# Optimization experiments

Hardware: AMD Instinct MI355X
Metric: run time of the kernel (lower is better)

## Reference

```python
import itertools
import jax, jax.numpy as jnp
import numpy as np

B, N, C, H = 4, 48, 16, 64
CIN = [48, 64, 128, 192]   # per-order MLP input dims after expand/reduce/concat/permute
COUT = 16

def _exclude_mask(n, cnt, dtype):
    # mask[i1..icnt] = 1 iff all object indices are pairwise distinct
    if cnt <= 1:
        return jnp.ones((n,), dtype=dtype)
    idx = [jnp.arange(n).reshape((1,) * d + (n,) + (1,) * (cnt - 1 - d)) for d in range(cnt)]
    m = jnp.ones((n,) * cnt, dtype=bool)
    for a in range(cnt):
        for b in range(a + 1, cnt):
            m = m & (idx[a] != idx[b])
    return m.astype(dtype)

def _reduce(x, dim):
    # x: [B] + [n]*dim + [C]; exists=max / forall=min over last object axis, exclude_self mask
    n = x.shape[1]
    m = _exclude_mask(n, dim, x.dtype)[..., None]  # [n]*dim + [1], broadcasts over B and C
    ex = jnp.max(x * m, axis=-2)
    fa = jnp.min(x * m + (1.0 - m), axis=-2)
    out = jnp.stack([ex, fa], axis=-1)  # interleave (exists, forall) per channel
    return out.reshape(out.shape[:-2] + (out.shape[-2] * 2,))

def _expand(x, dim, n):
    # insert a new object axis at position dim+1 and broadcast to n
    return jnp.broadcast_to(jnp.expand_dims(x, dim + 1), x.shape[:dim + 1] + (n,) + x.shape[dim + 1:])

def _permute(x, dim):
    # concat all permutations of the object axes along channels
    if dim <= 1:
        return x
    parts = [jnp.transpose(x, (0,) + p + (dim + 1,)) for p in itertools.permutations(range(1, dim + 1))]
    return jnp.concatenate(parts, axis=-1)

def _logic(x, W1, b1, W2, b2):
    # LogicInferenceLayer: Linear -> ReLU -> Linear -> Sigmoid on channel axis
    return jax.nn.sigmoid(jax.nn.relu(x @ W1 + b1) @ W2 + b2)

def setup_inputs() -> dict:
    key = jax.random.key(0)
    ks = jax.random.split(key, 24)
    inp = {
        'x0': jax.random.uniform(ks[0], (B, C), dtype=jnp.float32),
        'x1': jax.random.uniform(ks[1], (B, N, C), dtype=jnp.float32),
        'x2': jax.random.uniform(ks[2], (B, N, N, C), dtype=jnp.float32),
        'x3': jax.random.uniform(ks[3], (B, N, N, N, C), dtype=jnp.float32),
    }
    for o, cin in enumerate(CIN):
        inp[f'W1_{o}'] = jax.random.normal(ks[4 + 4 * o], (cin, H), dtype=jnp.float32) * 0.05
        inp[f'b1_{o}'] = jnp.zeros((H,), dtype=jnp.float32)
        inp[f'W2_{o}'] = jax.random.normal(ks[5 + 4 * o], (H, COUT), dtype=jnp.float32) * 0.05
        inp[f'b2_{o}'] = jnp.zeros((COUT,), dtype=jnp.float32)
    return inp

def reference(x0, x1, x2, x3,
              W1_0, b1_0, W2_0, b2_0,
              W1_1, b1_1, W2_1, b2_1,
              W1_2, b1_2, W2_2, b2_2,
              W1_3, b1_3, W2_3, b2_3):
    n = x1.shape[1]
    # order 0: [self, reduce(order1)]
    t0 = jnp.concatenate([x0, _reduce(x1, 1)], axis=-1)
    y0 = _logic(t0, W1_0, b1_0, W2_0, b2_0)
    # order 1: [expand(order0), self, reduce(order2)]
    t1 = jnp.concatenate([_expand(x0, 0, n), x1, _reduce(x2, 2)], axis=-1)
    y1 = _logic(t1, W1_1, b1_1, W2_1, b2_1)
    # order 2: [expand(order1), self, reduce(order3)], permute 2 object axes
    t2 = jnp.concatenate([_expand(x1, 1, n), x2, _reduce(x3, 3)], axis=-1)
    y2 = _logic(_permute(t2, 2), W1_2, b1_2, W2_2, b2_2)
    # order 3 (max order): [expand(order2), self], permute 3 object axes
    t3 = jnp.concatenate([_expand(x2, 2, n), x3], axis=-1)
    y3 = _logic(_permute(t3, 3), W1_3, b1_3, W2_3, b2_3)
    return (y0, y1, y2, y3)
```

## Files before the change

### kernel.cpp

```cpp
#include <hip/hip_runtime.h>
#include <hip/hip_bf16.h>


typedef __bf16 bf16x8 __attribute__((ext_vector_type(8)));
typedef unsigned short us8 __attribute__((ext_vector_type(8)));
typedef float f32x4 __attribute__((ext_vector_type(4)));

#define NPAIR 589824
#define NRED3 294912
#define NX3   7077888

__device__ __forceinline__ unsigned short f2bf(float f) {
    __hip_bfloat16 h = __float2bfloat16(f);
    return __builtin_bit_cast(unsigned short, h);
}
__device__ __forceinline__ unsigned int pk2(float a, float b) {
    return (unsigned int)f2bf(a) | ((unsigned int)f2bf(b) << 16);
}
__device__ __forceinline__ float bflo(unsigned int u) {
    return __builtin_bit_cast(float, u << 16);
}
__device__ __forceinline__ float bfhi(unsigned int u) {
    return __builtin_bit_cast(float, u & 0xffff0000u);
}
__device__ __forceinline__ float sigmoidf_(float z) {
    return 1.0f / (1.0f + __expf(-z));
}
__device__ __forceinline__ bf16x8 ld_bf8(const unsigned short* p) {
    return __builtin_bit_cast(bf16x8, *(const us8*)p);
}
__device__ __forceinline__ bf16x8 pack8(float4 a, float4 b) {
    us8 u;
    u[0] = f2bf(a.x); u[1] = f2bf(a.y); u[2] = f2bf(a.z); u[3] = f2bf(a.w);
    u[4] = f2bf(b.x); u[5] = f2bf(b.y); u[6] = f2bf(b.z); u[7] = f2bf(b.w);
    return __builtin_bit_cast(bf16x8, u);
}

__global__ __launch_bounds__(192) void perm3_kernel(
    const float* __restrict__ x3,
    unsigned short* __restrict__ X0, unsigned short* __restrict__ XA,
    unsigned short* __restrict__ XB, unsigned short* __restrict__ red3)
{
    __shared__ float rowf[768];
    const int g = blockIdx.x;
    const int m2 = g % 48, t1 = g / 48, m1 = t1 % 48, b = t1 / 48;
    const int t = threadIdx.x;
    const int m3 = t >> 2, cq = (t & 3) * 4;
    const float4 v = *(const float4*)(x3 + (size_t)g * 768 + m3 * 16 + cq);
    *(float4*)(rowf + m3 * 16 + cq) = v;
    const uint2 u = make_uint2(pk2(v.x, v.y), pk2(v.z, v.w));
    *(uint2*)(X0 + (size_t)g * 768 + m3 * 16 + cq) = u;
    *(uint2*)(XA + (((size_t)(b * 48 + m1) * 48 + m3) * 48 + m2) * 16 + cq) = u;
    *(uint2*)(XB + (((size_t)(b * 48 + m2) * 48 + m3) * 48 + m1) * 16 + cq) = u;
    __syncthreads();
    if (t < 16) {
        const int c = t;
        float ex = -__builtin_inff(), fa = __builtin_inff();
        const bool mij = (m1 != m2);
#pragma unroll 8
        for (int k = 0; k < 48; ++k) {
            const bool m = mij & (k != m1) & (k != m2);
            const float vv = rowf[k * 16 + c];
            ex = fmaxf(ex, m ? vv : 0.f);
            fa = fminf(fa, m ? vv : 1.f);
        }
        *(unsigned int*)(red3 + (size_t)g * 32 + 2 * c) = pk2(ex, fa);
    }
}

__global__ __launch_bounds__(256) void phaseA_kernel(
    const float* __restrict__ x2, const float* __restrict__ W1,
    const float* __restrict__ b1,
    float* __restrict__ wsA, unsigned short* __restrict__ wsB,
    unsigned short* __restrict__ wsC)
{
    __shared__ float xr[4][32];
    const int t = threadIdx.x;
    if (t < 128) {
        const int pr2 = t >> 5, c = t & 31;
        const int gg = blockIdx.x * 4 + pr2;
        const int bb = gg / 2304, pp2 = gg % 2304, P = pp2 / 48, Q = pp2 % 48;
        const float* base = x2 + (size_t)bb * 36864;
        xr[pr2][c] = (c < 16) ? base[(P * 48 + Q) * 16 + c]
                              : base[(Q * 48 + P) * 16 + (c - 16)];
    }
    __syncthreads();
    const int pr = t >> 6, h = t & 63;
    const int g = blockIdx.x * 4 + pr;
    float a = b1[h], bacc = 0.f, cacc = 0.f;
#pragma unroll
    for (int c = 0; c < 16; ++c) {
        const float xpq = xr[pr][c], xqp = xr[pr][16 + c];
        a    += xpq * W1[(  0 + c) * 64 + h] + xqp * W1[( 64 + c) * 64 + h];
        bacc += xpq * W1[( 32 + c) * 64 + h] + xqp * W1[( 96 + c) * 64 + h];
        cacc += xpq * W1[(128 + c) * 64 + h] + xqp * W1[(160 + c) * 64 + h];
    }
    const size_t o = (size_t)g * 64 + h;
    wsA[o] = a;
    wsB[o] = f2bf(bacc);
    wsC[o] = f2bf(cacc);
}

#define Y3_TILES 8

__global__ __launch_bounds__(192, 3) void y3_kernel(
    const unsigned short* __restrict__ X0,
    const unsigned short* __restrict__ XA,
    const unsigned short* __restrict__ XB,
    const float* __restrict__ W1, const float* __restrict__ W2,
    const float* __restrict__ b2,
    const float* __restrict__ wsA,
    const unsigned short* __restrict__ wsB,
    const unsigned short* __restrict__ wsC,
    float* __restrict__ out)
{
    __shared__ __align__(16) unsigned short w1t[64 * 104];
    const int t = threadIdx.x;
    const int w = t >> 6, lane = t & 63, lr = lane & 15, lg = lane >> 4;

#pragma unroll
    for (int p = 0; p < 16; ++p) {
        const int e = p * 192 + t;
        const int h = e & 63, kk = (e >> 6) * 2;
        const int r0 = 16 + ((kk >> 4) << 5) + (kk & 15);
        *(unsigned int*)(w1t + h * 104 + kk) =
            pk2(W1[r0 * 64 + h], W1[(r0 + 1) * 64 + h]);
    }
    __syncthreads();

    bf16x8 w1f[4][3];
#pragma unroll
    for (int n = 0; n < 4; ++n)
#pragma unroll
        for (int ks = 0; ks < 3; ++ks)
            w1f[n][ks] = ld_bf8(w1t + (16 * n + lr) * 104 + 32 * ks + 8 * lg);

    bf16x8 w2f[2];
#pragma unroll
    for (int m = 0; m < 2; ++m) {
        us8 u;
#pragma unroll
        for (int e = 0; e < 8; ++e) {
            const int ch = 16 * (e >> 1) + 4 * lg + 2 * (e & 1) + m;
            u[e] = f2bf(W2[ch * 16 + lr]);
        }
        w2f[m] = __builtin_bit_cast(bf16x8, u);
    }
    const float4 b2v = *(const float4*)(b2 + 4 * lg);
    const int row = 16 * w + lr;
    const int roff = row * 16 + 8 * (lg & 1);
    const bool hi = (lg >> 1) != 0;

    const int g0 = blockIdx.x * Y3_TILES;
    const int b = g0 / 2304, pp = g0 % 2304, i = pp / 48, j0 = pp % 48;

    const size_t baseB = ((size_t)((b * 48 + i) * 48 + row)) * 64 + 4 * lg;
    uint2 Bu[4];
#pragma unroll
    for (int n = 0; n < 4; ++n) Bu[n] = *(const uint2*)(wsB + baseB + 16 * n);

    const size_t rowIJ = ((size_t)(b * 48 + i) * 48) * 768;

    bf16x8 xc0, xc1, xc2;
    uint2 Cu[4];
    {
        const size_t bIJ = rowIJ + (size_t)j0 * 768;
        const size_t bJI = ((size_t)(b * 48 + j0) * 48 + i) * 768;
        xc0 = ld_bf8((hi ? XA + bIJ : X0 + bIJ) + roff);
        xc1 = ld_bf8((hi ? XB + bIJ : X0 + bJI) + roff);
        xc2 = ld_bf8((hi ? XB + bJI : XA + bJI) + roff);
        const size_t baseC = ((size_t)((b * 48 + j0) * 48 + row)) * 64 + 4 * lg;
#pragma unroll
        for (int n = 0; n < 4; ++n) Cu[n] = *(const uint2*)(wsC + baseC + 16 * n);
    }

#pragma unroll
    for (int it = 0; it < Y3_TILES; ++it) {
        const int j = j0 + it;
        bf16x8 xn0, xn1, xn2;
        uint2 Cn[4];
        if (it < Y3_TILES - 1) {
            const int jn = j + 1;
            const size_t bIJ = rowIJ + (size_t)jn * 768;
            const size_t bJI = ((size_t)(b * 48 + jn) * 48 + i) * 768;
            xn0 = ld_bf8((hi ? XA + bIJ : X0 + bIJ) + roff);
            xn1 = ld_bf8((hi ? XB + bIJ : X0 + bJI) + roff);
            xn2 = ld_bf8((hi ? XB + bJI : XA + bJI) + roff);
            const size_t baseC = ((size_t)((b * 48 + jn) * 48 + row)) * 64 + 4 * lg;
#pragma unroll
            for (int n = 0; n < 4; ++n) Cn[n] = *(const uint2*)(wsC + baseC + 16 * n);
        }
        f32x4 acc[4];
#pragma unroll
        for (int n = 0; n < 4; ++n) {
            acc[n] = f32x4{0.f, 0.f, 0.f, 0.f};
            acc[n] = __builtin_amdgcn_mfma_f32_16x16x32_bf16(w1f[n][0], xc0, acc[n], 0, 0, 0);
            acc[n] = __builtin_amdgcn_mfma_f32_16x16x32_bf16(w1f[n][1], xc1, acc[n], 0, 0, 0);
            acc[n] = __builtin_amdgcn_mfma_f32_16x16x32_bf16(w1f[n][2], xc2, acc[n], 0, 0, 0);
        }
        const size_t baseA = ((size_t)((b * 48 + i) * 48 + j)) * 64 + 4 * lg;
#pragma unroll
        for (int n = 0; n < 4; ++n) {
            const float4 Au = *(const float4*)(wsA + baseA + 16 * n);
            acc[n][0] = fmaxf(acc[n][0] + Au.x + bflo(Bu[n].x) + bflo(Cu[n].x), 0.f);
            acc[n][1] = fmaxf(acc[n][1] + Au.y + bfhi(Bu[n].x) + bfhi(Cu[n].x), 0.f);
            acc[n][2] = fmaxf(acc[n][2] + Au.z + bflo(Bu[n].y) + bflo(Cu[n].y), 0.f);
            acc[n][3] = fmaxf(acc[n][3] + Au.w + bfhi(Bu[n].y) + bfhi(Cu[n].y), 0.f);
        }
        bf16x8 hf[2];
#pragma unroll
        for (int m = 0; m < 2; ++m) {
            us8 u;
#pragma unroll
            for (int e = 0; e < 8; ++e)
                u[e] = f2bf(acc[e >> 1][2 * (e & 1) + m]);
            hf[m] = __builtin_bit_cast(bf16x8, u);
        }
        f32x4 o2 = {0.f, 0.f, 0.f, 0.f};
        o2 = __builtin_amdgcn_mfma_f32_16x16x32_bf16(w2f[0], hf[0], o2, 0, 0, 0);
        o2 = __builtin_amdgcn_mfma_f32_16x16x32_bf16(w2f[1], hf[1], o2, 0, 0, 0);
        float4 ov;
        ov.x = sigmoidf_(o2[0] + b2v.x);
        ov.y = sigmoidf_(o2[1] + b2v.y);
        ov.z = sigmoidf_(o2[2] + b2v.z);
        ov.w = sigmoidf_(o2[3] + b2v.w);
        *(float4*)(out + (size_t)(g0 + it) * 768 + row * 16 + 4 * lg) = ov;
        if (it < Y3_TILES - 1) {
            xc0 = xn0; xc1 = xn1; xc2 = xn2;
#pragma unroll
            for (int n = 0; n < 4; ++n) Cu[n] = Cn[n];
        }
    }
}

__global__ __launch_bounds__(192, 3) void y3_gather_kernel(
    const float* __restrict__ x3,
    const float* __restrict__ W1, const float* __restrict__ W2,
    const float* __restrict__ b2,
    const float* __restrict__ wsA,
    const unsigned short* __restrict__ wsB,
    const unsigned short* __restrict__ wsC,
    float* __restrict__ out)
{
    __shared__ __align__(16) unsigned short w1t[64 * 104];
    const int t = threadIdx.x;
    const int w = t >> 6, lane = t & 63, lr = lane & 15, lg = lane >> 4;
#pragma unroll
    for (int p = 0; p < 16; ++p) {
        const int e = p * 192 + t;
        const int h = e & 63, kk = (e >> 6) * 2;
        const int r0 = 16 + ((kk >> 4) << 5) + (kk & 15);
        *(unsigned int*)(w1t + h * 104 + kk) =
            pk2(W1[r0 * 64 + h], W1[(r0 + 1) * 64 + h]);
    }
    __syncthreads();
    bf16x8 w1f[4][3];
#pragma unroll
    for (int n = 0; n < 4; ++n)
#pragma unroll
        for (int ks = 0; ks < 3; ++ks)
            w1f[n][ks] = ld_bf8(w1t + (16 * n + lr) * 104 + 32 * ks + 8 * lg);
    bf16x8 w2f[2];
#pragma unroll
    for (int m = 0; m < 2; ++m) {
        us8 u;
// ... 65 lines not shown
        *(float4*)(out + (size_t)g * 768 + row * 16 + 4 * lg) = ov;
    }
}

__global__ __launch_bounds__(256) void red3_kernel(
    const float* __restrict__ x3, unsigned short* __restrict__ red3)
{
    const int slot = blockIdx.x * 256 + threadIdx.x;
    const int c = slot & 15;
    const int q = slot >> 4;
    const int j = q % 48, pi = q / 48, i = pi % 48;
    const float* p = x3 + (size_t)q * 768 + c;
    float ex = -__builtin_inff(), fa = __builtin_inff();
    const bool mij = (i != j);
#pragma unroll 8
    for (int k = 0; k < 48; ++k) {
        const bool m = mij & (k != i) & (k != j);
        const float v = p[k * 16];
        ex = fmaxf(ex, m ? v : 0.f);
        fa = fminf(fa, m ? v : 1.f);
    }
    *(unsigned int*)(red3 + (size_t)q * 32 + 2 * c) = pk2(ex, fa);
}

__global__ __launch_bounds__(192, 3) void y2_mlp_kernel(
    const float* __restrict__ x1, const float* __restrict__ x2,
    const float* __restrict__ W1, const float* __restrict__ b1,
    const float* __restrict__ W2, const float* __restrict__ b2,
    const unsigned short* __restrict__ red3, float* __restrict__ out)
{
    __shared__ __align__(16) unsigned short w1t[64 * 136];
    const int t = threadIdx.x;
    const int w = t >> 6, lane = t & 63, lr = lane & 15, lg = lane >> 4;

#pragma unroll
    for (int p = 0; p < 22; ++p) {
        const int e = p * 192 + t;
        if (e < 4096) {
            const int h = e & 63, k2 = e >> 6;
            *(unsigned int*)(w1t + h * 136 + 2 * k2) =
                pk2(W1[(2 * k2) * 64 + h], W1[(2 * k2 + 1) * 64 + h]);
        }
    }
    __syncthreads();

    bf16x8 w1f[4][4];
#pragma unroll
    for (int n = 0; n < 4; ++n)
#pragma unroll
        for (int ks = 0; ks < 4; ++ks)
            w1f[n][ks] = ld_bf8(w1t + (16 * n + lr) * 136 + 32 * ks + 8 * lg);

    bf16x8 w2f[2];
#pragma unroll
    for (int m = 0; m < 2; ++m) {
        us8 u;
#pragma unroll
        for (int e = 0; e < 8; ++e) {
            const int ch = 16 * (e >> 1) + 4 * lg + 2 * (e & 1) + m;
            u[e] = f2bf(W2[ch * 16 + lr]);
        }
        w2f[m] = __builtin_bit_cast(bf16x8, u);
    }
    float4 b1v[4];
#pragma unroll
    for (int n = 0; n < 4; ++n) b1v[n] = *(const float4*)(b1 + 16 * n + 4 * lg);
    const float4 b2v = *(const float4*)(b2 + 4 * lg);

    const int bq = blockIdx.x;
    const int b = bq / 48, i = bq % 48;
    const float* x2b = x2 + (size_t)b * 36864;
    const int row = 16 * w + lr;
    const int j = row;
    const int c0 = 8 * (lg & 1);
    const bool hi = (lg >> 1) != 0;

    const float* a0 = hi ? (x2b + (i * 48 + j) * 16 + c0) : (x1 + (b * 48 + i) * 16 + c0);
    const float* a2 = hi ? (x2b + (j * 48 + i) * 16 + c0) : (x1 + (b * 48 + j) * 16 + c0);
    const unsigned short* r1 = red3 + ((size_t)(b * 48 + i) * 48 + j) * 32 + (hi ? 16 : 0) + c0;
    const unsigned short* r3 = red3 + ((size_t)(b * 48 + j) * 48 + i) * 32 + (hi ? 16 : 0) + c0;

    const bf16x8 xf0 = pack8(*(const float4*)a0, *(const float4*)(a0 + 4));
    const bf16x8 xf1 = ld_bf8(r1);
    const bf16x8 xf2 = pack8(*(const float4*)a2, *(const float4*)(a2 + 4));
    const bf16x8 xf3 = ld_bf8(r3);

    f32x4 acc[4];
#pragma unroll
    for (int n = 0; n < 4; ++n) {
        acc[n] = f32x4{0.f, 0.f, 0.f, 0.f};
        acc[n] = __builtin_amdgcn_mfma_f32_16x16x32_bf16(w1f[n][0], xf0, acc[n], 0, 0, 0);
        acc[n] = __builtin_amdgcn_mfma_f32_16x16x32_bf16(w1f[n][1], xf1, acc[n], 0, 0, 0);
        acc[n] = __builtin_amdgcn_mfma_f32_16x16x32_bf16(w1f[n][2], xf2, acc[n], 0, 0, 0);
        acc[n] = __builtin_amdgcn_mfma_f32_16x16x32_bf16(w1f[n][3], xf3, acc[n], 0, 0, 0);
    }
#pragma unroll
    for (int n = 0; n < 4; ++n) {
        acc[n][0] = fmaxf(acc[n][0] + b1v[n].x, 0.f);
        acc[n][1] = fmaxf(acc[n][1] + b1v[n].y, 0.f);
        acc[n][2] = fmaxf(acc[n][2] + b1v[n].z, 0.f);
        acc[n][3] = fmaxf(acc[n][3] + b1v[n].w, 0.f);
    }
    bf16x8 hf[2];
#pragma unroll
    for (int m = 0; m < 2; ++m) {
        us8 u;
#pragma unroll
        for (int e = 0; e < 8; ++e)
            u[e] = f2bf(acc[e >> 1][2 * (e & 1) + m]);
        hf[m] = __builtin_bit_cast(bf16x8, u);
    }
    f32x4 o2 = {0.f, 0.f, 0.f, 0.f};
    o2 = __builtin_amdgcn_mfma_f32_16x16x32_bf16(w2f[0], hf[0], o2, 0, 0, 0);
    o2 = __builtin_amdgcn_mfma_f32_16x16x32_bf16(w2f[1], hf[1], o2, 0, 0, 0);
    float4 ov;
    ov.x = sigmoidf_(o2[0] + b2v.x);
    ov.y = sigmoidf_(o2[1] + b2v.y);
    ov.z = sigmoidf_(o2[2] + b2v.z);
    ov.w = sigmoidf_(o2[3] + b2v.w);
// ... 10 lines not shown
    float* __restrict__ out)
{
    const int t = threadIdx.x;
    if (blockIdx.x < 4) {
        __shared__ __align__(16) unsigned short w1t[64 * 72];
        __shared__ __align__(16) unsigned short red2l[48 * 32];
        const int b = blockIdx.x;
#pragma unroll
        for (int p = 0; p < 11; ++p) {
            const int e = p * 192 + t;
            if (e < 2048) {
                const int h = e & 63, k2 = e >> 6;
                *(unsigned int*)(w1t + h * 72 + 2 * k2) =
                    pk2(W1_1[(2 * k2) * 64 + h], W1_1[(2 * k2 + 1) * 64 + h]);
            }
        }
        const float* x2b = x2 + (size_t)b * 36864;
#pragma unroll
        for (int s4 = 0; s4 < 4; ++s4) {
            const int s = t + 192 * s4;
            const int i = s >> 4, c = s & 15;
            const float* p = x2b + i * 768 + c;
            float ex = -__builtin_inff(), fa = __builtin_inff();
#pragma unroll 8
            for (int jj = 0; jj < 48; ++jj) {
                const bool m = (jj != i);
                const float v = p[jj * 16];
                ex = fmaxf(ex, m ? v : 0.f);
                fa = fminf(fa, m ? v : 1.f);
            }
            *(unsigned int*)(red2l + i * 32 + 2 * c) = pk2(ex, fa);
        }
        __syncthreads();

        const int w = t >> 6, lane = t & 63, lr = lane & 15, lg = lane >> 4;
        const int i = 16 * w + lr;
        const int rho = b * 48 + i;
        bf16x8 w1f[4][2];
#pragma unroll
        for (int n = 0; n < 4; ++n)
#pragma unroll
            for (int ks = 0; ks < 2; ++ks)
                w1f[n][ks] = ld_bf8(w1t + (16 * n + lr) * 72 + 32 * ks + 8 * lg);
        bf16x8 w2f[2];
#pragma unroll
        for (int m = 0; m < 2; ++m) {
            us8 u;
#pragma unroll
            for (int e = 0; e < 8; ++e) {
                const int ch = 16 * (e >> 1) + 4 * lg + 2 * (e & 1) + m;
                u[e] = f2bf(W2_1[ch * 16 + lr]);
            }
            w2f[m] = __builtin_bit_cast(bf16x8, u);
        }
        float4 b1v[4];
#pragma unroll
        for (int n = 0; n < 4; ++n) b1v[n] = *(const float4*)(b1_1 + 16 * n + 4 * lg);
        const float4 b2v = *(const float4*)(b2_1 + 4 * lg);

        const int c0 = 8 * (lg & 1);
        const float* a0 = (lg < 2) ? (x0 + b * 16 + c0) : (x1 + rho * 16 + c0);
        const bf16x8 xf0 = pack8(*(const float4*)a0, *(const float4*)(a0 + 4));
        const bf16x8 xf1 = ld_bf8(red2l + i * 32 + 8 * lg);

        f32x4 acc[4];
#pragma unroll
        for (int n = 0; n < 4; ++n) {
            acc[n] = f32x4{0.f, 0.f, 0.f, 0.f};
            acc[n] = __builtin_amdgcn_mfma_f32_16x16x32_bf16(w1f[n][0], xf0, acc[n], 0, 0, 0);
            acc[n] = __builtin_amdgcn_mfma_f32_16x16x32_bf16(w1f[n][1], xf1, acc[n], 0, 0, 0);
        }
#pragma unroll
        for (int n = 0; n < 4; ++n) {
            acc[n][0] = fmaxf(acc[n][0] + b1v[n].x, 0.f);
            acc[n][1] = fmaxf(acc[n][1] + b1v[n].y, 0.f);
            acc[n][2] = fmaxf(acc[n][2] + b1v[n].z, 0.f);
            acc[n][3] = fmaxf(acc[n][3] + b1v[n].w, 0.f);
        }
        bf16x8 hf[2];
#pragma unroll
        for (int m = 0; m < 2; ++m) {
            us8 u;
#pragma unroll
            for (int e = 0; e < 8; ++e)
                u[e] = f2bf(acc[e >> 1][2 * (e & 1) + m]);
            hf[m] = __builtin_bit_cast(bf16x8, u);
        }
        f32x4 o2 = {0.f, 0.f, 0.f, 0.f};
        o2 = __builtin_amdgcn_mfma_f32_16x16x32_bf16(w2f[0], hf[0], o2, 0, 0, 0);
        o2 = __builtin_amdgcn_mfma_f32_16x16x32_bf16(w2f[1], hf[1], o2, 0, 0, 0);
        float4 ov;
        ov.x = sigmoidf_(o2[0] + b2v.x);
        ov.y = sigmoidf_(o2[1] + b2v.y);
        ov.z = sigmoidf_(o2[2] + b2v.z);
        ov.w = sigmoidf_(o2[3] + b2v.w);
        *(float4*)(out + 64 + (size_t)rho * 16 + 4 * lg) = ov;
    } else {
// ... 230 lines not shown
extern "C" void kernel_launch(void* const* d_in, const int* in_sizes, int n_in,
                              void* d_out, int out_size, void* d_ws, size_t ws_size,
                              hipStream_t stream) {
    (void)in_sizes; (void)n_in; (void)out_size;
    const float* x0 = (const float*)d_in[0];
    const float* x1 = (const float*)d_in[1];
    const float* x2 = (const float*)d_in[2];
    const float* x3 = (const float*)d_in[3];
    const float* W1_0 = (const float*)d_in[4];
    const float* b1_0 = (const float*)d_in[5];
    const float* W2_0 = (const float*)d_in[6];
    const float* b2_0 = (const float*)d_in[7];
    const float* W1_1 = (const float*)d_in[8];
    const float* b1_1 = (const float*)d_in[9];
    const float* W2_1 = (const float*)d_in[10];
    const float* b2_1 = (const float*)d_in[11];
    const float* W1_2 = (const float*)d_in[12];
    const float* b1_2 = (const float*)d_in[13];
    const float* W2_2 = (const float*)d_in[14];
    const float* b2_2 = (const float*)d_in[15];
    const float* W1_3 = (const float*)d_in[16];
    const float* b1_3 = (const float*)d_in[17];
    const float* W2_3 = (const float*)d_in[18];
    const float* b2_3 = (const float*)d_in[19];
    float* out = (float*)d_out;

    const size_t ws_mid  = (size_t)8 * NPAIR + (size_t)2 * NRED3;
    const size_t ws_full = ws_mid + (size_t)6 * NX3;
    if (ws_size >= ws_mid) {
        float* wsA = (float*)d_ws;
        unsigned short* wsB = (unsigned short*)d_ws + 2 * NPAIR;
        unsigned short* wsC = wsB + NPAIR;
        unsigned short* red3 = (unsigned short*)d_ws + 4 * NPAIR;
        phaseA_kernel<<<2304, 256, 0, stream>>>(x2, W1_3, b1_3, wsA, wsB, wsC);
        if (ws_size >= ws_full) {
            unsigned short* X0 = red3 + NRED3;
            unsigned short* XA = X0 + NX3;
            unsigned short* XB = XA + NX3;
            perm3_kernel<<<9216, 192, 0, stream>>>(x3, X0, XA, XB, red3);
            y3_kernel<<<9216 / Y3_TILES, 192, 0, stream>>>(
                X0, XA, XB, W1_3, W2_3, b2_3, wsA, wsB, wsC, out + 150592);
        } else {
            y3_gather_kernel<<<2304, 192, 0, stream>>>(x3, W1_3, W2_3, b2_3,
                                                       wsA, wsB, wsC, out + 150592);
            red3_kernel<<<576, 256, 0, stream>>>(x3, red3);
        }
        y2_mlp_kernel<<<192, 192, 0, stream>>>(x1, x2, W1_2, b1_2, W2_2, b2_2,
                                               red3, out + 3136);
    } else {
        y3_fallback_kernel<<<1024, 192, 0, stream>>>(x2, x3, W1_3, b1_3, W2_3, b2_3,
                                                     out + 150592);
        y2_kernel<<<192, 192, 0, stream>>>(x1, x2, x3, W1_2, b1_2, W2_2, b2_2,
                                           out + 3136);
    }
    y01_kernel<<<5, 192, 0, stream>>>(x0, x1, x2, W1_0, b1_0, W2_0, b2_0,
                                      W1_1, b1_1, W2_1, b2_1, out);
}
```

Before: 184.0 us.

## Merge five launches into two heterogeneous kernels with parallel reduce and prefetched wsA

```diff
diff --git a/kernel.cpp b/kernel.cpp
--- a/kernel.cpp
+++ b/kernel.cpp
@@ -9,6 +9,7 @@
 #define NPAIR 589824
 #define NRED3 294912
 #define NX3   7077888
+#define Y3_TILES 8
 
 __device__ __forceinline__ unsigned short f2bf(float f) {
     __hip_bfloat16 h = __float2bfloat16(f);
@@ -36,35 +37,455 @@
     return __builtin_bit_cast(bf16x8, u);
 }
 
-__global__ __launch_bounds__(192) void perm3_kernel(
-    const float* __restrict__ x3,
+__global__ __launch_bounds__(256) void pre_kernel(
+    const float* __restrict__ x2, const float* __restrict__ x3,
+    const float* __restrict__ W1, const float* __restrict__ b1,
+    float* __restrict__ wsA, unsigned short* __restrict__ wsB,
+    unsigned short* __restrict__ wsC,
     unsigned short* __restrict__ X0, unsigned short* __restrict__ XA,
     unsigned short* __restrict__ XB, unsigned short* __restrict__ red3)
 {
+    __shared__ float xr[4][32];
     __shared__ float rowf[768];
-    const int g = blockIdx.x;
-    const int m2 = g % 48, t1 = g / 48, m1 = t1 % 48, b = t1 / 48;
+    __shared__ float pex[12][16];
+    __shared__ float pfa[12][16];
     const int t = threadIdx.x;
-    const int m3 = t >> 2, cq = (t & 3) * 4;
-    const float4 v = *(const float4*)(x3 + (size_t)g * 768 + m3 * 16 + cq);
-    *(float4*)(rowf + m3 * 16 + cq) = v;
-    const uint2 u = make_uint2(pk2(v.x, v.y), pk2(v.z, v.w));
-    *(uint2*)(X0 + (size_t)g * 768 + m3 * 16 + cq) = u;
-    *(uint2*)(XA + (((size_t)(b * 48 + m1) * 48 + m3) * 48 + m2) * 16 + cq) = u;
-    *(uint2*)(XB + (((size_t)(b * 48 + m2) * 48 + m3) * 48 + m1) * 16 + cq) = u;
-    __syncthreads();
-    if (t < 16) {
-        const int c = t;
-        float ex = -__builtin_inff(), fa = __builtin_inff();
+
+    if (blockIdx.x < 2304) {
+        if (t < 128) {
+            const int pr2 = t >> 5, c = t & 31;
+            const int gg = blockIdx.x * 4 + pr2;
+            const int bb = gg / 2304, pp2 = gg % 2304, P = pp2 / 48, Q = pp2 % 48;
+            const float* base = x2 + (size_t)bb * 36864;
+            xr[pr2][c] = (c < 16) ? base[(P * 48 + Q) * 16 + c]
+                                  : base[(Q * 48 + P) * 16 + (c - 16)];
+        }
+        __syncthreads();
+        const int pr = t >> 6, h = t & 63;
+        const int g = blockIdx.x * 4 + pr;
+        float a = b1[h], bacc = 0.f, cacc = 0.f;
+#pragma unroll
+        for (int c = 0; c < 16; ++c) {
+            const float xpq = xr[pr][c], xqp = xr[pr][16 + c];
+            a    += xpq * W1[(  0 + c) * 64 + h] + xqp * W1[( 64 + c) * 64 + h];
+            bacc += xpq * W1[( 32 + c) * 64 + h] + xqp * W1[( 96 + c) * 64 + h];
+            cacc += xpq * W1[(128 + c) * 64 + h] + xqp * W1[(160 + c) * 64 + h];
+        }
+        const size_t o = (size_t)g * 64 + h;
+        wsA[o] = a;
+        wsB[o] = f2bf(bacc);
+        wsC[o] = f2bf(cacc);
+    } else {
+        const int g = blockIdx.x - 2304;
+        const int m2 = g % 48, t1 = g / 48, m1 = t1 % 48, b = t1 / 48;
+        if (t < 192) {
+            const int m3 = t >> 2, cq = (t & 3) * 4;
+            const float4 v = *(const float4*)(x3 + (size_t)g * 768 + m3 * 16 + cq);
+            *(float4*)(rowf + m3 * 16 + cq) = v;
+            const uint2 u = make_uint2(pk2(v.x, v.y), pk2(v.z, v.w));
+            *(uint2*)(X0 + (size_t)g * 768 + m3 * 16 + cq) = u;
+            *(uint2*)(XA + (((size_t)(b * 48 + m1) * 48 + m3) * 48 + m2) * 16 + cq) = u;
+            *(uint2*)(XB + (((size_t)(b * 48 + m2) * 48 + m3) * 48 + m1) * 16 + cq) = u;
+        }
+        __syncthreads();
         const bool mij = (m1 != m2);
+        if (t < 192) {
+            const int kk = t >> 4, c = t & 15;
+            float ex = -__builtin_inff(), fa = __builtin_inff();
+#pragma unroll
+            for (int k4 = 0; k4 < 4; ++k4) {
+                const int k = kk * 4 + k4;
+                const bool m = mij & (k != m1) & (k != m2);
+                const float vv = rowf[k * 16 + c];
+                ex = fmaxf(ex, m ? vv : 0.f);
+                fa = fminf(fa, m ? vv : 1.f);
+            }
+            pex[kk][c] = ex;
+            pfa[kk][c] = fa;
+        }
+        __syncthreads();
+        if (t < 16) {
+            const int c = t;
+            float ex = -__builtin_inff(), fa = __builtin_inff();
+#pragma unroll
+            for (int kk = 0; kk < 12; ++kk) {
+                ex = fmaxf(ex, pex[kk][c]);
+                fa = fminf(fa, pfa[kk][c]);
+            }
+            *(unsigned int*)(red3 + (size_t)g * 32 + 2 * c) = pk2(ex, fa);
+        }
+    }
+}
+
+__global__ __launch_bounds__(192, 3) void main_kernel(
+    const unsigned short* __restrict__ X0,
+    const unsigned short* __restrict__ XA,
+    const unsigned short* __restrict__ XB,
+    const float* __restrict__ W1_3, const float* __restrict__ W2_3,
+    const float* __restrict__ b2_3,
+    const float* __restrict__ wsA,
+    const unsigned short* __restrict__ wsB,
+    const unsigned short* __restrict__ wsC,
+    const float* __restrict__ x1, const float* __restrict__ x2,
+    const float* __restrict__ W1_2, const float* __restrict__ b1_2,
+    const float* __restrict__ W2_2, const float* __restrict__ b2_2,
+    const unsigned short* __restrict__ red3,
+    const float* __restrict__ x0,
+    const float* __restrict__ W1_0, const float* __restrict__ b1_0,
+    const float* __restrict__ W2_0, const float* __restrict__ b2_0,
+    const float* __restrict__ W1_1, const float* __restrict__ b1_1,
+    const float* __restrict__ W2_1, const float* __restrict__ b2_1,
+    float* __restrict__ out)
+{
+    __shared__ __align__(16) unsigned short w1t[64 * 136];
+    __shared__ __align__(16) unsigned short red2l[48 * 32];
+    __shared__ float t0l[4][56];
+    __shared__ float hl[4][72];
+    const int t = threadIdx.x;
+    const int w = t >> 6, lane = t & 63, lr = lane & 15, lg = lane >> 4;
+
+    if (blockIdx.x < 1152) {
+        float* y3out = out + 150592;
+#pragma unroll
+        for (int p = 0; p < 16; ++p) {
+            const int e = p * 192 + t;
+            const int h = e & 63, kk = (e >> 6) * 2;
+            const int r0 = 16 + ((kk >> 4) << 5) + (kk & 15);
+            *(unsigned int*)(w1t + h * 104 + kk) =
+                pk2(W1_3[r0 * 64 + h], W1_3[(r0 + 1) * 64 + h]);
+        }
+        __syncthreads();
+
+        bf16x8 w1f[4][3];
+#pragma unroll
+        for (int n = 0; n < 4; ++n)
+#pragma unroll
+            for (int ks = 0; ks < 3; ++ks)
+                w1f[n][ks] = ld_bf8(w1t + (16 * n + lr) * 104 + 32 * ks + 8 * lg);
+
+        bf16x8 w2f[2];
+#pragma unroll
+        for (int m = 0; m < 2; ++m) {
+            us8 u;
+#pragma unroll
+            for (int e = 0; e < 8; ++e) {
+                const int ch = 16 * (e >> 1) + 4 * lg + 2 * (e & 1) + m;
+                u[e] = f2bf(W2_3[ch * 16 + lr]);
+            }
+            w2f[m] = __builtin_bit_cast(bf16x8, u);
+        }
+        const float4 b2v = *(const float4*)(b2_3 + 4 * lg);
+        const int row = 16 * w + lr;
+        const int roff = row * 16 + 8 * (lg & 1);
+        const bool hi = (lg >> 1) != 0;
+
+        const int g0 = blockIdx.x * Y3_TILES;
+        const int b = g0 / 2304, pp = g0 % 2304, i = pp / 48, j0 = pp % 48;
+
+        const size_t baseB = ((size_t)((b * 48 + i) * 48 + row)) * 64 + 4 * lg;
+        uint2 Bu[4];
+#pragma unroll
+        for (int n = 0; n < 4; ++n) Bu[n] = *(const uint2*)(wsB + baseB + 16 * n);
+
+        const size_t rowIJ = ((size_t)(b * 48 + i) * 48) * 768;
+
+        bf16x8 xc0, xc1, xc2;
+        uint2 Cu[4];
+        float4 Av[4];
+        {
+            const size_t bIJ = rowIJ + (size_t)j0 * 768;
+            const size_t bJI = ((size_t)(b * 48 + j0) * 48 + i) * 768;
+            xc0 = ld_bf8((hi ? XA + bIJ : X0 + bIJ) + roff);
+            xc1 = ld_bf8((hi ? XB + bIJ : X0 + bJI) + roff);
+            xc2 = ld_bf8((hi ? XB + bJI : XA + bJI) + roff);
+            const size_t baseC = ((size_t)((b * 48 + j0) * 48 + row)) * 64 + 4 * lg;
+            const size_t baseA = ((size_t)((b * 48 + i) * 48 + j0)) * 64 + 4 * lg;
+#pragma unroll
+            for (int n = 0; n < 4; ++n) {
+                Cu[n] = *(const uint2*)(wsC + baseC + 16 * n);
+                Av[n] = *(const float4*)(wsA + baseA + 16 * n);
+            }
+        }
+
+#pragma unroll
+        for (int it = 0; it < Y3_TILES; ++it) {
+            const int j = j0 + it;
+            bf16x8 xn0, xn1, xn2;
+            uint2 Cn[4];
+            float4 An[4];
+            if (it < Y3_TILES - 1) {
+                const int jn = j + 1;
+                const size_t bIJ = rowIJ + (size_t)jn * 768;
+                const size_t bJI = ((size_t)(b * 48 + jn) * 48 + i) * 768;
+                xn0 = ld_bf8((hi ? XA + bIJ : X0 + bIJ) + roff);
+                xn1 = ld_bf8((hi ? XB + bIJ : X0 + bJI) + roff);
+                xn2 = ld_bf8((hi ? XB + bJI : XA + bJI) + roff);
+                const size_t baseC = ((size_t)((b * 48 + jn) * 48 + row)) * 64 + 4 * lg;
+                const size_t baseA = ((size_t)((b * 48 + i) * 48 + jn)) * 64 + 4 * lg;
+#pragma unroll
+                for (int n = 0; n < 4; ++n) {
+                    Cn[n] = *(const uint2*)(wsC + baseC + 16 * n);
+                    An[n] = *(const float4*)(wsA + baseA + 16 * n);
+                }
+            }
+            f32x4 acc[4];
+#pragma unroll
+            for (int n = 0; n < 4; ++n) {
+                acc[n] = f32x4{0.f, 0.f, 0.f, 0.f};
+                acc[n] = __builtin_amdgcn_mfma_f32_16x16x32_bf16(w1f[n][0], xc0, acc[n], 0, 0, 0);
+                acc[n] = __builtin_amdgcn_mfma_f32_16x16x32_bf16(w1f[n][1], xc1, acc[n], 0, 0, 0);
+                acc[n] = __builtin_amdgcn_mfma_f32_16x16x32_bf16(w1f[n][2], xc2, acc[n], 0, 0, 0);
+            }
+#pragma unroll
+            for (int n = 0; n < 4; ++n) {
+                acc[n][0] = fmaxf(acc[n][0] + Av[n].x + bflo(Bu[n].x) + bflo(Cu[n].x), 0.f);
+                acc[n][1] = fmaxf(acc[n][1] + Av[n].y + bfhi(Bu[n].x) + bfhi(Cu[n].x), 0.f);
+                acc[n][2] = fmaxf(acc[n][2] + Av[n].z + bflo(Bu[n].y) + bflo(Cu[n].y), 0.f);
+                acc[n][3] = fmaxf(acc[n][3] + Av[n].w + bfhi(Bu[n].y) + bfhi(Cu[n].y), 0.f);
+            }
+            bf16x8 hf[2];
+#pragma unroll
+            for (int m = 0; m < 2; ++m) {
+                us8 u;
+#pragma unroll
+                for (int e = 0; e < 8; ++e)
+                    u[e] = f2bf(acc[e >> 1][2 * (e & 1) + m]);
+                hf[m] = __builtin_bit_cast(bf16x8, u);
+            }
+            f32x4 o2 = {0.f, 0.f, 0.f, 0.f};
+            o2 = __builtin_amdgcn_mfma_f32_16x16x32_bf16(w2f[0], hf[0], o2, 0, 0, 0);
+            o2 = __builtin_amdgcn_mfma_f32_16x16x32_bf16(w2f[1], hf[1], o2, 0, 0, 0);
+            float4 ov;
+            ov.x = sigmoidf_(o2[0] + b2v.x);
+            ov.y = sigmoidf_(o2[1] + b2v.y);
+            ov.z = sigmoidf_(o2[2] + b2v.z);
+            ov.w = sigmoidf_(o2[3] + b2v.w);
+            *(float4*)(y3out + (size_t)(g0 + it) * 768 + row * 16 + 4 * lg) = ov;
+            if (it < Y3_TILES - 1) {
+                xc0 = xn0; xc1 = xn1; xc2 = xn2;
+#pragma unroll
+                for (int n = 0; n < 4; ++n) { Cu[n] = Cn[n]; Av[n] = An[n]; }
+            }
+        }
+    } else if (blockIdx.x < 1344) {
+        float* y2out = out + 3136;
+#pragma unroll
+        for (int p = 0; p < 22; ++p) {
+            const int e = p * 192 + t;
+            if (e < 4096) {
+                const int h = e & 63, k2 = e >> 6;
+                *(unsigned int*)(w1t + h * 136 + 2 * k2) =
+                    pk2(W1_2[(2 * k2) * 64 + h], W1_2[(2 * k2 + 1) * 64 + h]);
+            }
+        }
+        __syncthreads();
+
+        bf16x8 w1f[4][4];
+#pragma unroll
+        for (int n = 0; n < 4; ++n)
+#pragma unroll
+            for (int ks = 0; ks < 4; ++ks)
+                w1f[n][ks] = ld_bf8(w1t + (16 * n + lr) * 136 + 32 * ks + 8 * lg);
+
+        bf16x8 w2f[2];
+#pragma unroll
+        for (int m = 0; m < 2; ++m) {
+            us8 u;
+#pragma unroll
+            for (int e = 0; e < 8; ++e) {
+                const int ch = 16 * (e >> 1) + 4 * lg + 2 * (e & 1) + m;
+                u[e] = f2bf(W2_2[ch * 16 + lr]);
+            }
+            w2f[m] = __builtin_bit_cast(bf16x8, u);
+        }
+        float4 b1v[4];
+#pragma unroll
+        for (int n = 0; n < 4; ++n) b1v[n] = *(const float4*)(b1_2 + 16 * n + 4 * lg);
+        const float4 b2v = *(const float4*)(b2_2 + 4 * lg);
+
+        const int bq = blockIdx.x - 1152;
+        const int b = bq / 48, i = bq % 48;
+        const float* x2b = x2 + (size_t)b * 36864;
+        const int row = 16 * w + lr;
+        const int j = row;
+        const int c0 = 8 * (lg & 1);
+        const bool hi = (lg >> 1) != 0;
+
+        const float* a0 = hi ? (x2b + (i * 48 + j) * 16 + c0) : (x1 + (b * 48 + i) * 16 + c0);
+        const float* a2 = hi ? (x2b + (j * 48 + i) * 16 + c0) : (x1 + (b * 48 + j) * 16 + c0);
+        const unsigned short* r1 = red3 + ((size_t)(b * 48 + i) * 48 + j) * 32 + (hi ? 16 : 0) + c0;
+        const unsigned short* r3 = red3 + ((size_t)(b * 48 + j) * 48 + i) * 32 + (hi ? 16 : 0) + c0;
+
+        const bf16x8 xf0 = pack8(*(const float4*)a0, *(const float4*)(a0 + 4));
+        const bf16x8 xf1 = ld_bf8(r1);
+        const bf16x8 xf2 = pack8(*(const float4*)a2, *(const float4*)(a2 + 4));
+        const bf16x8 xf3 = ld_bf8(r3);
+
+        f32x4 acc[4];
+#pragma unroll
+        for (int n = 0; n < 4; ++n) {
+            acc[n] = f32x4{0.f, 0.f, 0.f, 0.f};
+            acc[n] = __builtin_amdgcn_mfma_f32_16x16x32_bf16(w1f[n][0], xf0, acc[n], 0, 0, 0);
+            acc[n] = __builtin_amdgcn_mfma_f32_16x16x32_bf16(w1f[n][1], xf1, acc[n], 0, 0, 0);
+            acc[n] = __builtin_amdgcn_mfma_f32_16x16x32_bf16(w1f[n][2], xf2, acc[n], 0, 0, 0);
+            acc[n] = __builtin_amdgcn_mfma_f32_16x16x32_bf16(w1f[n][3], xf3, acc[n], 0, 0, 0);
+        }
+#pragma unroll
+        for (int n = 0; n < 4; ++n) {
+            acc[n][0] = fmaxf(acc[n][0] + b1v[n].x, 0.f);
+            acc[n][1] = fmaxf(acc[n][1] + b1v[n].y, 0.f);
+            acc[n][2] = fmaxf(acc[n][2] + b1v[n].z, 0.f);
+            acc[n][3] = fmaxf(acc[n][3] + b1v[n].w, 0.f);
+        }
+        bf16x8 hf[2];
+#pragma unroll
+        for (int m = 0; m < 2; ++m) {
+            us8 u;
+#pragma unroll
+            for (int e = 0; e < 8; ++e)
+                u[e] = f2bf(acc[e >> 1][2 * (e & 1) + m]);
+            hf[m] = __builtin_bit_cast(bf16x8, u);
+        }
+        f32x4 o2 = {0.f, 0.f, 0.f, 0.f};
+        o2 = __builtin_amdgcn_mfma_f32_16x16x32_bf16(w2f[0], hf[0], o2, 0, 0, 0);
+        o2 = __builtin_amdgcn_mfma_f32_16x16x32_bf16(w2f[1], hf[1], o2, 0, 0, 0);
+        float4 ov;
+        ov.x = sigmoidf_(o2[0] + b2v.x);
+        ov.y = sigmoidf_(o2[1] + b2v.y);
+        ov.z = sigmoidf_(o2[2] + b2v.z);
+        ov.w = sigmoidf_(o2[3] + b2v.w);
+        *(float4*)(y2out + ((size_t)bq * 48 + row) * 16 + 4 * lg) = ov;
+    } else if (blockIdx.x < 1348) {
+        const int b = blockIdx.x - 1344;
+#pragma unroll
+        for (int p = 0; p < 11; ++p) {
+            const int e = p * 192 + t;
+            if (e < 2048) {
+                const int h = e & 63, k2 = e >> 6;
+                *(unsigned int*)(w1t + h * 72 + 2 * k2) =
+                    pk2(W1_1[(2 * k2) * 64 + h], W1_1[(2 * k2 + 1) * 64 + h]);
+            }
+        }
+        const float* x2b = x2 + (size_t)b * 36864;
+#pragma unroll
+        for (int s4 = 0; s4 < 4; ++s4) {
+            const int s = t + 192 * s4;
+            const int i = s >> 4, c = s & 15;
+            const float* p = x2b + i * 768 + c;
+            float ex = -__builtin_inff(), fa = __builtin_inff();
 #pragma unroll 8
-        for (int k = 0; k < 48; ++k) {
-            const bool m = mij & (k != m1) & (k != m2);
-            const float vv = rowf[k * 16 + c];
-            ex = fmaxf(ex, m ? vv : 0.f);
-            fa = fminf(fa, m ? vv : 1.f);
-        }
-        *(unsigned int*)(red3 + (size_t)g * 32 + 2 * c) = pk2(ex, fa);
+            for (int jj = 0; jj < 48; ++jj) {
+                const bool m = (jj != i);
+                const float v = p[jj * 16];
+                ex = fmaxf(ex, m ? v : 0.f);
+                fa = fminf(fa, m ? v : 1.f);
+            }
+            *(unsigned int*)(red2l + i * 32 + 2 * c) = pk2(ex, fa);
+        }
+        __syncthreads();
+
+        const int i = 16 * w + lr;
+        const int rho = b * 48 + i;
+        bf16x8 w1f[4][2];
+#pragma unroll
+        for (int n = 0; n < 4; ++n)
+#pragma unroll
+            for (int ks = 0; ks < 2; ++ks)
+                w1f[n][ks] = ld_bf8(w1t + (16 * n + lr) * 72 + 32 * ks + 8 * lg);
+        bf16x8 w2f[2];
+#pragma unroll
+        for (int m = 0; m < 2; ++m) {
+            us8 u;
+#pragma unroll
+            for (int e = 0; e < 8; ++e) {
+                const int ch = 16 * (e >> 1) + 4 * lg + 2 * (e & 1) + m;
+                u[e] = f2bf(W2_1[ch * 16 + lr]);
+            }
+            w2f[m] = __builtin_bit_cast(bf16x8, u);
+        }
+        float4 b1v[4];
+#pragma unroll
+        for (int n = 0; n < 4; ++n) b1v[n] = *(const float4*)(b1_1 + 16 * n + 4 * lg);
+        const float4 b2v = *(const float4*)(b2_1 + 4 * lg);
+
+        const int c0 = 8 * (lg & 1);
+        const float* a0 = (lg < 2) ? (x0 + b * 16 + c0) : (x1 + rho * 16 + c0);
+        const bf16x8 xf0 = pack8(*(const float4*)a0, *(const float4*)(a0 + 4));
+        const bf16x8 xf1 = ld_bf8(red2l + i * 32 + 8 * lg);
+
+        f32x4 acc[4];
+#pragma unroll
+        for (int n = 0; n < 4; ++n) {
+            acc[n] = f32x4{0.f, 0.f, 0.f, 0.f};
+            acc[n] = __builtin_amdgcn_mfma_f32_16x16x32_bf16(w1f[n][0], xf0, acc[n], 0, 0, 0);
+            acc[n] = __builtin_amdgcn_mfma_f32_16x16x32_bf16(w1f[n][1], xf1, acc[n], 0, 0, 0);
+        }
+#pragma unroll
+        for (int n = 0; n < 4; ++n) {
+            acc[n][0] = fmaxf(acc[n][0] + b1v[n].x, 0.f);
+            acc[n][1] = fmaxf(acc[n][1] + b1v[n].y, 0.f);
+            acc[n][2] = fmaxf(acc[n][2] + b1v[n].z, 0.f);
+            acc[n][3] = fmaxf(acc[n][3] + b1v[n].w, 0.f);
+        }
+        bf16x8 hf[2];
+#pragma unroll
+        for (int m = 0; m < 2; ++m) {
+            us8 u;
+#pragma unroll
+            for (int e = 0; e < 8; ++e)
+                u[e] = f2bf(acc[e >> 1][2 * (e & 1) + m]);
+            hf[m] = __builtin_bit_cast(bf16x8, u);
+        }
+        f32x4 o2 = {0.f, 0.f, 0.f, 0.f};
+        o2 = __builtin_amdgcn_mfma_f32_16x16x32_bf16(w2f[0], hf[0], o2, 0, 0, 0);
+        o2 = __builtin_amdgcn_mfma_f32_16x16x32_bf16(w2f[1], hf[1], o2, 0, 0, 0);
+        float4 ov;
+        ov.x = sigmoidf_(o2[0] + b2v.x);
+        ov.y = sigmoidf_(o2[1] + b2v.y);
+        ov.z = sigmoidf_(o2[2] + b2v.z);
+        ov.w = sigmoidf_(o2[3] + b2v.w);
+        *(float4*)(out + 64 + (size_t)rho * 16 + 4 * lg) = ov;
+    } else {
+        if (t < 64) {
+            const int b = t >> 4, c = t & 15;
+            const float* p = x1 + b * 768 + c;
+            float ex = -__builtin_inff(), fa = __builtin_inff();
+#pragma unroll 8
+            for (int n = 0; n < 48; ++n) {
+                const float v = p[n * 16];
+                ex = fmaxf(ex, v);
+                fa = fminf(fa, v);
+            }
+            t0l[b][c] = x0[b * 16 + c];
+            t0l[b][16 + 2 * c] = ex;
+            t0l[b][17 + 2 * c] = fa;
+        }
+        __syncthreads();
+        if (t < 64) {
+            const int h = t;
+            float ac0 = b1_0[h], ac1 = ac0, ac2 = ac0, ac3 = ac0;
+#pragma unroll
+            for (int c = 0; c < 48; ++c) {
+                const float wv = W1_0[c * 64 + h];
+                ac0 = fmaf(t0l[0][c], wv, ac0);
+                ac1 = fmaf(t0l[1][c], wv, ac1);
+                ac2 = fmaf(t0l[2][c], wv, ac2);
+                ac3 = fmaf(t0l[3][c], wv, ac3);
+            }
+            hl[0][h] = fmaxf(ac0, 0.f);
+            hl[1][h] = fmaxf(ac1, 0.f);
+            hl[2][h] = fmaxf(ac2, 0.f);
+            hl[3][h] = fmaxf(ac3, 0.f);
+        }
+        __syncthreads();
+        if (t < 64) {
+            const int b = t >> 4, o = t & 15;
+            float a = b2_0[o];
+#pragma unroll
+            for (int h = 0; h < 64; ++h)
+                a = fmaf(hl[b][h], W2_0[h * 16 + o], a);
+            out[b * 16 + o] = sigmoidf_(a);
+        }
     }
 }
 
@@ -99,138 +520,6 @@
     wsA[o] = a;
     wsB[o] = f2bf(bacc);
     wsC[o] = f2bf(cacc);
-}
-
-#define Y3_TILES 8
-
-__global__ __launch_bounds__(192, 3) void y3_kernel(
-    const unsigned short* __restrict__ X0,
-    const unsigned short* __restrict__ XA,
-    const unsigned short* __restrict__ XB,
-    const float* __restrict__ W1, const float* __restrict__ W2,
-    const float* __restrict__ b2,
-    const float* __restrict__ wsA,
-    const unsigned short* __restrict__ wsB,
-    const unsigned short* __restrict__ wsC,
-    float* __restrict__ out)
-{
-    __shared__ __align__(16) unsigned short w1t[64 * 104];
-    const int t = threadIdx.x;
-    const int w = t >> 6, lane = t & 63, lr = lane & 15, lg = lane >> 4;
-
-#pragma unroll
-    for (int p = 0; p < 16; ++p) {
-        const int e = p * 192 + t;
-        const int h = e & 63, kk = (e >> 6) * 2;
-        const int r0 = 16 + ((kk >> 4) << 5) + (kk & 15);
-        *(unsigned int*)(w1t + h * 104 + kk) =
-            pk2(W1[r0 * 64 + h], W1[(r0 + 1) * 64 + h]);
-    }
-    __syncthreads();
-
-    bf16x8 w1f[4][3];
-#pragma unroll
-    for (int n = 0; n < 4; ++n)
-#pragma unroll
-        for (int ks = 0; ks < 3; ++ks)
-            w1f[n][ks] = ld_bf8(w1t + (16 * n + lr) * 104 + 32 * ks + 8 * lg);
-
-    bf16x8 w2f[2];
-#pragma unroll
-    for (int m = 0; m < 2; ++m) {
-        us8 u;
-#pragma unroll
-        for (int e = 0; e < 8; ++e) {
-            const int ch = 16 * (e >> 1) + 4 * lg + 2 * (e & 1) + m;
-            u[e] = f2bf(W2[ch * 16 + lr]);
-        }
-        w2f[m] = __builtin_bit_cast(bf16x8, u);
-    }
-    const float4 b2v = *(const float4*)(b2 + 4 * lg);
-    const int row = 16 * w + lr;
-    const int roff = row * 16 + 8 * (lg & 1);
-    const bool hi = (lg >> 1) != 0;
-
-    const int g0 = blockIdx.x * Y3_TILES;
-    const int b = g0 / 2304, pp = g0 % 2304, i = pp / 48, j0 = pp % 48;
-
-    const size_t baseB = ((size_t)((b * 48 + i) * 48 + row)) * 64 + 4 * lg;
-    uint2 Bu[4];
-#pragma unroll
-    for (int n = 0; n < 4; ++n) Bu[n] = *(const uint2*)(wsB + baseB + 16 * n);
-
-    const size_t rowIJ = ((size_t)(b * 48 + i) * 48) * 768;
-
-    bf16x8 xc0, xc1, xc2;
-    uint2 Cu[4];
-    {
-        const size_t bIJ = rowIJ + (size_t)j0 * 768;
-        const size_t bJI = ((size_t)(b * 48 + j0) * 48 + i) * 768;
-        xc0 = ld_bf8((hi ? XA + bIJ : X0 + bIJ) + roff);
-        xc1 = ld_bf8((hi ? XB + bIJ : X0 + bJI) + roff);
-        xc2 = ld_bf8((hi ? XB + bJI : XA + bJI) + roff);
-        const size_t baseC = ((size_t)((b * 48 + j0) * 48 + row)) * 64 + 4 * lg;
-#pragma unroll
-        for (int n = 0; n < 4; ++n) Cu[n] = *(const uint2*)(wsC + baseC + 16 * n);
-    }
-
-#pragma unroll
-    for (int it = 0; it < Y3_TILES; ++it) {
-        const int j = j0 + it;
-        bf16x8 xn0, xn1, xn2;
-        uint2 Cn[4];
-        if (it < Y3_TILES - 1) {
-            const int jn = j + 1;
-            const size_t bIJ = rowIJ + (size_t)jn * 768;
-            const size_t bJI = ((size_t)(b * 48 + jn) * 48 + i) * 768;
-            xn0 = ld_bf8((hi ? XA + bIJ : X0 + bIJ) + roff);
-            xn1 = ld_bf8((hi ? XB + bIJ : X0 + bJI) + roff);
-            xn2 = ld_bf8((hi ? XB + bJI : XA + bJI) + roff);
-            const size_t baseC = ((size_t)((b * 48 + jn) * 48 + row)) * 64 + 4 * lg;
-#pragma unroll
-            for (int n = 0; n < 4; ++n) Cn[n] = *(const uint2*)(wsC + baseC + 16 * n);
-        }
-        f32x4 acc[4];
-#pragma unroll
-        for (int n = 0; n < 4; ++n) {
-            acc[n] = f32x4{0.f, 0.f, 0.f, 0.f};
-            acc[n] = __builtin_amdgcn_mfma_f32_16x16x32_bf16(w1f[n][0], xc0, acc[n], 0, 0, 0);
-            acc[n] = __builtin_amdgcn_mfma_f32_16x16x32_bf16(w1f[n][1], xc1, acc[n], 0, 0, 0);
-            acc[n] = __builtin_amdgcn_mfma_f32_16x16x32_bf16(w1f[n][2], xc2, acc[n], 0, 0, 0);
-        }
-        const size_t baseA = ((size_t)((b * 48 + i) * 48 + j)) * 64 + 4 * lg;
-#pragma unroll
-        for (int n = 0; n < 4; ++n) {
-            const float4 Au = *(const float4*)(wsA + baseA + 16 * n);
-            acc[n][0] = fmaxf(acc[n][0] + Au.x + bflo(Bu[n].x) + bflo(Cu[n].x), 0.f);
-            acc[n][1] = fmaxf(acc[n][1] + Au.y + bfhi(Bu[n].x) + bfhi(Cu[n].x), 0.f);
-            acc[n][2] = fmaxf(acc[n][2] + Au.z + bflo(Bu[n].y) + bflo(Cu[n].y), 0.f);
-            acc[n][3] = fmaxf(acc[n][3] + Au.w + bfhi(Bu[n].y) + bfhi(Cu[n].y), 0.f);
-        }
-        bf16x8 hf[2];
-#pragma unroll
-        for (int m = 0; m < 2; ++m) {
-            us8 u;
-#pragma unroll
-            for (int e = 0; e < 8; ++e)
-                u[e] = f2bf(acc[e >> 1][2 * (e & 1) + m]);
-            hf[m] = __builtin_bit_cast(bf16x8, u);
-        }
-        f32x4 o2 = {0.f, 0.f, 0.f, 0.f};
-        o2 = __builtin_amdgcn_mfma_f32_16x16x32_bf16(w2f[0], hf[0], o2, 0, 0, 0);
-        o2 = __builtin_amdgcn_mfma_f32_16x16x32_bf16(w2f[1], hf[1], o2, 0, 0, 0);
-        float4 ov;
-        ov.x = sigmoidf_(o2[0] + b2v.x);
-        ov.y = sigmoidf_(o2[1] + b2v.y);
-        ov.z = sigmoidf_(o2[2] + b2v.z);
-        ov.w = sigmoidf_(o2[3] + b2v.w);
-        *(float4*)(out + (size_t)(g0 + it) * 768 + row * 16 + 4 * lg) = ov;
-        if (it < Y3_TILES - 1) {
-            xc0 = xn0; xc1 = xn1; xc2 = xn2;
-#pragma unroll
-            for (int n = 0; n < 4; ++n) Cu[n] = Cn[n];
-        }
-    }
 }
 
 __global__ __launch_bounds__(192, 3) void y3_gather_kernel(
@@ -362,7 +651,6 @@
     __shared__ __align__(16) unsigned short w1t[64 * 136];
     const int t = threadIdx.x;
     const int w = t >> 6, lane = t & 63, lr = lane & 15, lg = lane >> 4;
-
 #pragma unroll
     for (int p = 0; p < 22; ++p) {
         const int e = p * 192 + t;
@@ -373,14 +661,12 @@
         }
     }
     __syncthreads();
-
     bf16x8 w1f[4][4];
 #pragma unroll
     for (int n = 0; n < 4; ++n)
 #pragma unroll
         for (int ks = 0; ks < 4; ++ks)
             w1f[n][ks] = ld_bf8(w1t + (16 * n + lr) * 136 + 32 * ks + 8 * lg);
-
     bf16x8 w2f[2];
 #pragma unroll
     for (int m = 0; m < 2; ++m) {
@@ -396,7 +682,6 @@
 #pragma unroll
     for (int n = 0; n < 4; ++n) b1v[n] = *(const float4*)(b1 + 16 * n + 4 * lg);
     const float4 b2v = *(const float4*)(b2 + 4 * lg);
-
     const int bq = blockIdx.x;
     const int b = bq / 48, i = bq % 48;
     const float* x2b = x2 + (size_t)b * 36864;
@@ -404,17 +689,14 @@
     const int j = row;
     const int c0 = 8 * (lg & 1);
     const bool hi = (lg >> 1) != 0;
-
     const float* a0 = hi ? (x2b + (i * 48 + j) * 16 + c0) : (x1 + (b * 48 + i) * 16 + c0);
     const float* a2 = hi ? (x2b + (j * 48 + i) * 16 + c0) : (x1 + (b * 48 + j) * 16 + c0);
     const unsigned short* r1 = red3 + ((size_t)(b * 48 + i) * 48 + j) * 32 + (hi ? 16 : 0) + c0;
     const unsigned short* r3 = red3 + ((size_t)(b * 48 + j) * 48 + i) * 32 + (hi ? 16 : 0) + c0;
-
     const bf16x8 xf0 = pack8(*(const float4*)a0, *(const float4*)(a0 + 4));
     const bf16x8 xf1 = ld_bf8(r1);
     const bf16x8 xf2 = pack8(*(const float4*)a2, *(const float4*)(a2 + 4));
     const bf16x8 xf3 = ld_bf8(r3);
-
     f32x4 acc[4];
 #pragma unroll
     for (int n = 0; n < 4; ++n) {
@@ -491,7 +773,6 @@
             *(unsigned int*)(red2l + i * 32 + 2 * c) = pk2(ex, fa);
         }
         __syncthreads();
-
         const int w = t >> 6, lane = t & 63, lr = lane & 15, lg = lane >> 4;
         const int i = 16 * w + lr;
         const int rho = b * 48 + i;
@@ -516,12 +797,10 @@
 #pragma unroll
         for (int n = 0; n < 4; ++n) b1v[n] = *(const float4*)(b1_1 + 16 * n + 4 * lg);
         const float4 b2v = *(const float4*)(b2_1 + 4 * lg);
-
         const int c0 = 8 * (lg & 1);
         const float* a0 = (lg < 2) ? (x0 + b * 16 + c0) : (x1 + rho * 16 + c0);
         const bf16x8 xf0 = pack8(*(const float4*)a0, *(const float4*)(a0 + 4));
         const bf16x8 xf1 = ld_bf8(red2l + i * 32 + 8 * lg);
-
         f32x4 acc[4];
 #pragma unroll
         for (int n = 0; n < 4; ++n) {
@@ -818,27 +1097,33 @@
         unsigned short* wsB = (unsigned short*)d_ws + 2 * NPAIR;
         unsigned short* wsC = wsB + NPAIR;
         unsigned short* red3 = (unsigned short*)d_ws + 4 * NPAIR;
-        phaseA_kernel<<<2304, 256, 0, stream>>>(x2, W1_3, b1_3, wsA, wsB, wsC);
         if (ws_size >= ws_full) {
             unsigned short* X0 = red3 + NRED3;
             unsigned short* XA = X0 + NX3;
             unsigned short* XB = XA + NX3;
-            perm3_kernel<<<9216, 192, 0, stream>>>(x3, X0, XA, XB, red3);
-            y3_kernel<<<9216 / Y3_TILES, 192, 0, stream>>>(
-                X0, XA, XB, W1_3, W2_3, b2_3, wsA, wsB, wsC, out + 150592);
+            pre_kernel<<<11520, 256, 0, stream>>>(x2, x3, W1_3, b1_3,
+                                                  wsA, wsB, wsC, X0, XA, XB, red3);
+            main_kernel<<<1349, 192, 0, stream>>>(X0, XA, XB, W1_3, W2_3, b2_3,
+                                                  wsA, wsB, wsC,
+                                                  x1, x2, W1_2, b1_2, W2_2, b2_2, red3,
+                                                  x0, W1_0, b1_0, W2_0, b2_0,
+                                                  W1_1, b1_1, W2_1, b2_1, out);
         } else {
+            phaseA_kernel<<<2304, 256, 0, stream>>>(x2, W1_3, b1_3, wsA, wsB, wsC);
             y3_gather_kernel<<<2304, 192, 0, stream>>>(x3, W1_3, W2_3, b2_3,
                                                        wsA, wsB, wsC, out + 150592);
             red3_kernel<<<576, 256, 0, stream>>>(x3, red3);
-        }
-        y2_mlp_kernel<<<192, 192, 0, stream>>>(x1, x2, W1_2, b1_2, W2_2, b2_2,
-                                               red3, out + 3136);
+            y2_mlp_kernel<<<192, 192, 0, stream>>>(x1, x2, W1_2, b1_2, W2_2, b2_2,
+                                                   red3, out + 3136);
+            y01_kernel<<<5, 192, 0, stream>>>(x0, x1, x2, W1_0, b1_0, W2_0, b2_0,
+                                              W1_1, b1_1, W2_1, b2_1, out);
+        }
     } else {
         y3_fallback_kernel<<<1024, 192, 0, stream>>>(x2, x3, W1_3, b1_3, W2_3, b2_3,
                                                      out + 150592);
         y2_kernel<<<192, 192, 0, stream>>>(x1, x2, x3, W1_2, b1_2, W2_2, b2_2,
                                            out + 3136);
-    }
-    y01_kernel<<<5, 192, 0, stream>>>(x0, x1, x2, W1_0, b1_0, W2_0, b2_0,
-                                      W1_1, b1_1, W2_1, b2_1, out);
-}
+        y01_kernel<<<5, 192, 0, stream>>>(x0, x1, x2, W1_0, b1_0, W2_0, b2_0,
+                                          W1_1, b1_1, W2_1, b2_1, out);
+    }
+}
```

Result: faster. 166.8 us (-9.4%).
